# Kernel tuning notes

Hardware: AMD Instinct MI355X
Metric: run time of the kernel (lower is better)

Reference implementation:

```python
import jax, jax.numpy as jnp
import numpy as np

CLASSES = (32, 32)
SUPERCLASSES = 8
OVERALL = CLASSES[0] * CLASSES[1]
CLASS_FACTOR = OVERALL // SUPERCLASSES


def lrelu(x):
    return jax.nn.leaky_relu(x, 0.01)


def conv1x1(x, w, b):
    # x: [B,C,H,W], w: [O,C], b: [O]
    return jnp.einsum('oc,bchw->bohw', w, x) + b[None, :, None, None]


def cond_mul(x, inds, W, b):
    # x: [N,I], inds: [N] int, W: [K,I,O], b: [K,O]
    return jnp.einsum('ni,nio->no', x, W[inds]) + b[inds]


def setup_inputs() -> dict:
    key = jax.random.key(0)
    ks = jax.random.split(key, 24)
    s = 0.05
    d = {}
    d['x_in'] = jax.random.normal(ks[0], (1, 128, 192, 256), dtype=jnp.float32)
    # mask branch
    d['Wm1'] = jax.random.normal(ks[1], (32, 128)) * s
    d['bm1'] = jnp.zeros((32,), jnp.float32)
    d['Wm2'] = jax.random.normal(ks[2], (16, 32)) * s
    d['bm2'] = jnp.zeros((16,), jnp.float32)
    d['Wm3'] = jax.random.normal(ks[3], (1, 16)) * s
    d['bm3'] = jnp.zeros((1,), jnp.float32)
    # classification branch
    d['Wcl1'] = jax.random.normal(ks[4], (128, 128)) * s
    d['bcl1'] = jnp.zeros((128,), jnp.float32)
    d['Wcl21'] = jax.random.normal(ks[5], (128, 128)) * s
    d['bcl21'] = jnp.zeros((128,), jnp.float32)
    d['Wcl31'] = jax.random.normal(ks[6], (32, 128)) * s
    d['bcl31'] = jnp.zeros((32,), jnp.float32)
    d['Wcl22'] = jax.random.normal(ks[7], (CLASSES[0], 128, 32)) * s  # CondMul
    d['bcl22'] = jnp.zeros((CLASSES[0], 32), jnp.float32)
    d['Wcl32'] = jax.random.normal(ks[8], (CLASSES[0], 32, CLASSES[1])) * s
    d['bcl32'] = jnp.zeros((CLASSES[0], CLASSES[1]), jnp.float32)
    d['Wr1'] = jax.random.normal(ks[9], (128, 128)) * s
    d['br1'] = jnp.zeros((128,), jnp.float32)
    d['Wr2'] = jax.random.normal(ks[10], (SUPERCLASSES, 128, 32)) * s
    d['br2'] = jnp.zeros((SUPERCLASSES, 32), jnp.float32)
    d['Wr3'] = jax.random.normal(ks[11], (OVERALL, 32, 1)) * s
    d['br3'] = jnp.zeros((OVERALL, 1), jnp.float32)
    return d


def reference(x_in, Wm1, bm1, Wm2, bm2, Wm3, bm3,
              Wcl1, bcl1, Wcl21, bcl21, Wcl31, bcl31,
              Wcl22, bcl22, Wcl32, bcl32,
              Wr1, br1, Wr2, br2, Wr3, br3):
    B = x_in.shape[0]
    # mask branch
    m = lrelu(conv1x1(x_in, Wm1, bm1))
    m = lrelu(conv1x1(m, Wm2, bm2))
    mask = lrelu(conv1x1(m, Wm3, bm3))
    # classification branch
    x = lrelu(conv1x1(x_in, Wcl1, bcl1))          # [B,128,H,W]
    # torch: transpose(1,3) -> [B,W,H,C], flatten
    x_l = jnp.transpose(x, (0, 3, 2, 1)).reshape(-1, x.shape[1])
    x2 = lrelu(conv1x1(x, Wcl21, bcl21))
    cl1 = conv1x1(x2, Wcl31, bcl31)               # [B,classes0,H,W]
    inds1 = jnp.argmax(cl1, axis=1).reshape(-1).astype(jnp.int32)  # [N] (B,H,W order)
    h = lrelu(cond_mul(x_l, inds1, Wcl22, bcl22))  # [N,32]
    h = cond_mul(h, inds1, Wcl32, bcl32)           # [N,classes1]
    inds2 = jnp.argmax(h, axis=1).astype(jnp.int32)
    inds = inds1 * CLASSES[1] + inds2
    inds_r = jnp.clip(inds, 0, OVERALL - 1).astype(jnp.int32)
    inds_super = jnp.clip(inds_r // CLASS_FACTOR, 0, SUPERCLASSES - 1)
    r = lrelu(conv1x1(x_in, Wr1, br1))
    r_l = jnp.transpose(r, (0, 3, 2, 1)).reshape(-1, r.shape[1])
    r2 = lrelu(cond_mul(r_l, inds_super, Wr2, br2))  # [N,32]
    regression = cond_mul(r2, inds_r, Wr3, br3)      # [N,1]
    regression = regression.reshape(B, 1, 1, -1)
    inds = inds.reshape(regression.shape)
    x_real = (inds.astype(jnp.float32) + regression) * (1.0 / float(OVERALL))
    return (x_real, mask)
```

## Files before the change

### kernel.cpp

```cpp
#include <hip/hip_runtime.h>

#define HH 192
#define WW 256
#define NPIX (HH*WW)
#define NSEG (NPIX/64)

__device__ __forceinline__ float lrelu(float v) { return v > 0.0f ? v : 0.01f * v; }

__global__ __launch_bounds__(256, 3) void k_fused1(
    const float* __restrict__ X,
    const float* __restrict__ Wcl1, const float* __restrict__ bcl1,
    const float* __restrict__ Wr1,  const float* __restrict__ br1,
    const float* __restrict__ Wm1,  const float* __restrict__ bm1,
    const float* __restrict__ Wm2,  const float* __restrict__ bm2,
    const float* __restrict__ Wm3,  const float* __restrict__ bm3,
    float* __restrict__ x_t, float* __restrict__ r_t,
    float* __restrict__ out)
{
    __shared__ float As[16][132];
    __shared__ float Ws[16][132];
    __shared__ float m1buf[128][33];
    const int tid = threadIdx.x;
    const int q0  = blockIdx.x * 128;

    if (blockIdx.y == 2) {
        const int tc = tid & 31;
        const int tr = tid >> 5;
        float acc[4][4];
        #pragma unroll
        for (int i = 0; i < 4; ++i)
            #pragma unroll
            for (int j = 0; j < 4; ++j)
                acc[i][j] = bm1[tr * 4 + j];

        for (int k0 = 0; k0 < 128; k0 += 16) {
            #pragma unroll
            for (int p = 0; p < 2; ++p) {
                int lin = p * 1024 + tid * 4;
                int kk = lin >> 7, px = lin & 127;
                float4 v = *(const float4*)(X + (k0 + kk) * NPIX + q0 + px);
                *(float4*)(&As[kk][px]) = v;
            }
            if (tid < 128) {
                int row = tid >> 2, kc = (tid & 3) * 4;
                float4 v = *(const float4*)(Wm1 + row * 128 + k0 + kc);
                Ws[kc + 0][row] = v.x; Ws[kc + 1][row] = v.y;
                Ws[kc + 2][row] = v.z; Ws[kc + 3][row] = v.w;
            }
            __syncthreads();
            #pragma unroll
            for (int kk = 0; kk < 16; ++kk) {
                float4 a = *(const float4*)(&As[kk][tc * 4]);
                float4 w = *(const float4*)(&Ws[kk][tr * 4]);
                float av[4] = {a.x,a.y,a.z,a.w};
                float wv[4] = {w.x,w.y,w.z,w.w};
                #pragma unroll
                for (int i = 0; i < 4; ++i)
                    #pragma unroll
                    for (int j = 0; j < 4; ++j)
                        acc[i][j] = fmaf(av[i], wv[j], acc[i][j]);
            }
            __syncthreads();
        }
        #pragma unroll
        for (int i = 0; i < 4; ++i)
            #pragma unroll
            for (int j = 0; j < 4; ++j)
                m1buf[tc * 4 + i][tr * 4 + j] = lrelu(acc[i][j]);
        __syncthreads();
        if (tid < 128) {
            float m3 = bm3[0];
            #pragma unroll 2
            for (int j = 0; j < 16; ++j) {
                float s = bm2[j];
                #pragma unroll
                for (int k = 0; k < 32; ++k)
                    s = fmaf(Wm2[j * 32 + k], m1buf[tid][k], s);
                m3 = fmaf(Wm3[j], lrelu(s), m3);
            }
            out[NPIX + q0 + tid] = lrelu(m3);
        }
        return;
    }

    const float* __restrict__ W    = (blockIdx.y == 0) ? Wcl1 : Wr1;
    const float* __restrict__ bias = (blockIdx.y == 0) ? bcl1 : br1;
    float* __restrict__ outp       = (blockIdx.y == 0) ? x_t : r_t;

    const int tc = tid & 15;
    const int tr = tid >> 4;

    float acc[8][8];
    #pragma unroll
    for (int i = 0; i < 8; ++i)
        #pragma unroll
        for (int j = 0; j < 8; ++j)
            acc[i][j] = bias[(j >> 2) * 64 + tr * 4 + (j & 3)];

    for (int k0 = 0; k0 < 128; k0 += 16) {
        #pragma unroll
        for (int p = 0; p < 2; ++p) {
            int lin = p * 1024 + tid * 4;
            int kk = lin >> 7, px = lin & 127;
            float4 v = *(const float4*)(X + (k0 + kk) * NPIX + q0 + px);
            *(float4*)(&As[kk][px]) = v;
        }
        #pragma unroll
        for (int p = 0; p < 2; ++p) {
            int lin = p * 1024 + tid * 4;
            int row = lin >> 4, kc = lin & 15;
            float4 v = *(const float4*)(W + row * 128 + k0 + kc);
            Ws[kc + 0][row] = v.x; Ws[kc + 1][row] = v.y;
            Ws[kc + 2][row] = v.z; Ws[kc + 3][row] = v.w;
        }
        __syncthreads();
        #pragma unroll
        for (int kk = 0; kk < 16; ++kk) {
            float4 a0 = *(const float4*)(&As[kk][tc * 4]);
            float4 a1 = *(const float4*)(&As[kk][64 + tc * 4]);
            float4 w0 = *(const float4*)(&Ws[kk][tr * 4]);
            float4 w1 = *(const float4*)(&Ws[kk][64 + tr * 4]);
            float av[8] = {a0.x,a0.y,a0.z,a0.w,a1.x,a1.y,a1.z,a1.w};
            float wv[8] = {w0.x,w0.y,w0.z,w0.w,w1.x,w1.y,w1.z,w1.w};
            #pragma unroll
            for (int i = 0; i < 8; ++i)
                #pragma unroll
                for (int j = 0; j < 8; ++j)
                    acc[i][j] = fmaf(av[i], wv[j], acc[i][j]);
        }
        __syncthreads();
    }

    #pragma unroll
    for (int i = 0; i < 8; ++i) {
        int px = (i >> 2) * 64 + tc * 4 + (i & 3);
        int q  = q0 + px;
        int np = (q & 255) * 192 + (q >> 8);
        float* op = outp + (size_t)np * 128;
        #pragma unroll
        for (int jg = 0; jg < 2; ++jg) {
            float4 o;
            o.x = lrelu(acc[i][jg*4+0]); o.y = lrelu(acc[i][jg*4+1]);
            o.z = lrelu(acc[i][jg*4+2]); o.w = lrelu(acc[i][jg*4+3]);
            *(float4*)(op + jg * 64 + tr * 4) = o;
        }
    }
}

__global__ __launch_bounds__(256, 3) void k1b(
    const float* __restrict__ x_t,
    const float* __restrict__ Wcl21, const float* __restrict__ bcl21,
    const float* __restrict__ Wcl31, const float* __restrict__ bcl31,
    int* __restrict__ inds1_q)
{
    __shared__ float smem[8576];
    float (*As)[132]    = (float(*)[132])smem;
    float (*Ws)[132]    = (float(*)[132])(smem + 2112);
    float (*W31)[132]   = (float(*)[132])smem;
    float (*x2t)[68]    = (float(*)[68])(smem + 4224);
    float (*cl1buf)[33] = (float(*)[33])(smem + 4224);

    const int tid = threadIdx.x;
    const int n0  = blockIdx.x * 64;
    const int tcA = tid & 15, trA = tid >> 4;

    float acc[4][8];
    #pragma unroll
    for (int i = 0; i < 4; ++i)
        #pragma unroll
        for (int j = 0; j < 8; ++j)
            acc[i][j] = bcl21[(j >> 2) * 64 + trA * 4 + (j & 3)];

    for (int k0 = 0; k0 < 128; k0 += 16) {
        {
            int lin = tid * 4;
            int px = lin >> 4, kc = lin & 15;
            float4 v = *(const float4*)(x_t + (size_t)(n0 + px) * 128 + k0 + kc);
            As[kc + 0][px] = v.x; As[kc + 1][px] = v.y;
            As[kc + 2][px] = v.z; As[kc + 3][px] = v.w;
        }
        #pragma unroll
        for (int p = 0; p < 2; ++p) {
            int lin = p * 256 + tid;
            int r = lin >> 2, kc = (lin & 3) * 4;
            float4 v = *(const float4*)(Wcl21 + r * 128 + k0 + kc);
            Ws[kc + 0][r] = v.x; Ws[kc + 1][r] = v.y;
            Ws[kc + 2][r] = v.z; Ws[kc + 3][r] = v.w;
        }
        __syncthreads();
        #pragma unroll
        for (int kk = 0; kk < 16; ++kk) {
            float4 a  = *(const float4*)(&As[kk][tcA * 4]);
            float4 w0 = *(const float4*)(&Ws[kk][trA * 4]);
            float4 w1 = *(const float4*)(&Ws[kk][64 + trA * 4]);
            float av[4] = {a.x,a.y,a.z,a.w};
            float wv[8] = {w0.x,w0.y,w0.z,w0.w,w1.x,w1.y,w1.z,w1.w};
            #pragma unroll
            for (int i = 0; i < 4; ++i)
                #pragma unroll
                for (int j = 0; j < 8; ++j)
                    acc[i][j] = fmaf(av[i], wv[j], acc[i][j]);
        }
        __syncthreads();
    }

    const int tcB = tid & 15;
    const int trB = tid >> 4;
    float accB[4][2];
    #pragma unroll
    for (int i = 0; i < 4; ++i)
        #pragma unroll
        for (int j = 0; j < 2; ++j)
            accB[i][j] = bcl31[trB * 2 + j];

    #pragma unroll
    for (int p = 0; p < 4; ++p) {
        int lin = p * 1024 + tid * 4;
        int row = lin >> 7, kc = lin & 127;
        *(float4*)(&W31[row][kc]) = *(const float4*)(Wcl31 + row * 128 + kc);
    }
    #pragma unroll
    for (int j = 0; j < 4; ++j) {
        float4 o;
        o.x = lrelu(acc[0][j]); o.y = lrelu(acc[1][j]);
        o.z = lrelu(acc[2][j]); o.w = lrelu(acc[3][j]);
        *(float4*)(&x2t[trA * 4 + j][tcA * 4]) = o;
    }
    __syncthreads();
    for (int k = 0; k < 64; ++k) {
        float4 a = *(const float4*)(&x2t[k][tcB * 4]);
        float av[4] = {a.x,a.y,a.z,a.w};
        float w0 = W31[trB * 2 + 0][k];
        float w1 = W31[trB * 2 + 1][k];
        #pragma unroll
        for (int i = 0; i < 4; ++i) {
            accB[i][0] = fmaf(av[i], w0, accB[i][0]);
            accB[i][1] = fmaf(av[i], w1, accB[i][1]);
        }
    }
    __syncthreads();
    #pragma unroll
    for (int j = 0; j < 4; ++j) {
        float4 o;
        o.x = lrelu(acc[0][4+j]); o.y = lrelu(acc[1][4+j]);
        o.z = lrelu(acc[2][4+j]); o.w = lrelu(acc[3][4+j]);
        *(float4*)(&x2t[trA * 4 + j][tcA * 4]) = o;
    }
    __syncthreads();
    for (int k = 0; k < 64; ++k) {
        float4 a = *(const float4*)(&x2t[k][tcB * 4]);
        float av[4] = {a.x,a.y,a.z,a.w};
        float w0 = W31[trB * 2 + 0][64 + k];
        float w1 = W31[trB * 2 + 1][64 + k];
        #pragma unroll
        for (int i = 0; i < 4; ++i) {
            accB[i][0] = fmaf(av[i], w0, accB[i][0]);
            accB[i][1] = fmaf(av[i], w1, accB[i][1]);
        }
    }
    __syncthreads();

    #pragma unroll
    for (int i = 0; i < 4; ++i)
        #pragma unroll
        for (int j = 0; j < 2; ++j)
            cl1buf[tcB * 4 + i][trB * 2 + j] = accB[i][j];
    __syncthreads();
    if (tid < 64) {
        float bv = cl1buf[tid][0]; int bi = 0;
        #pragma unroll
        for (int c = 1; c < 32; ++c) {
            float v = cl1buf[tid][c];
            if (v > bv) { bv = v; bi = c; }
        }
        int n = n0 + tid;
        int w = n / 192, hh = n - w * 192;
        inds1_q[hh * 256 + w] = bi;
    }
}

__global__ void k_hist(const int* __restrict__ inds1_q, int* __restrict__ bh) {
    int tid = threadIdx.x;
    int n = blockIdx.x * 256 + tid;
    int key = inds1_q[n];
    int lane = tid & 63;
    int cnt = 0;
    for (int k = 0; k < 32; ++k) {
        unsigned long long m = __ballot(key == k);
        if (lane == k) cnt = __popcll(m);
    }
    if (lane < 32) bh[(n >> 6) * 32 + lane] = cnt;
}

__global__ void k_scanA(const int* __restrict__ bh, int* __restrict__ ebb,
                        int* __restrict__ total) {
    __shared__ int s[256];
    const int k = blockIdx.x, t = threadIdx.x;
    int v0 = bh[(t * 3 + 0) * 32 + k];
    int v1 = bh[(t * 3 + 1) * 32 + k];
    int v2 = bh[(t * 3 + 2) * 32 + k];
    int sum = v0 + v1 + v2;
    s[t] = sum; __syncthreads();
    for (int d = 1; d < 256; d <<= 1) {
        int x = (t >= d) ? s[t - d] : 0;
        __syncthreads();
        s[t] += x;
        __syncthreads();
    }
    int ex = s[t] - sum;
    ebb[(t * 3 + 0) * 32 + k] = ex;
    ebb[(t * 3 + 1) * 32 + k] = ex + v0;
    ebb[(t * 3 + 2) * 32 + k] = ex + v0 + v1;
    if (t == 255) total[k] = s[255];
}

__global__ void k_scatter2(const int* __restrict__ inds1_q,
                           const int* __restrict__ ebb,
                           const int* __restrict__ total,
                           int* __restrict__ order)
{
    __shared__ int ttot[32];
    const int tid = threadIdx.x;
    if (tid < 32) ttot[tid] = total[tid];
    __syncthreads();
    int n = blockIdx.x * 256 + tid;
    int key = inds1_q[n];
    int lane = tid & 63;
    unsigned long long peers = 0;
    for (int k = 0; k < 32; ++k) {
        unsigned long long m = __ballot(key == k);
        if (key == k) peers = m;
    }
    int rank = __popcll(peers & ((1ull << lane) - 1ull));
    int cbase = 0;
    #pragma unroll
    for (int k = 0; k < 32; ++k) cbase += (k < key) ? ttot[k] : 0;
    order[cbase + ebb[(n >> 6) * 32 + key] + rank] = n;
}

__global__ __launch_bounds__(256, 4) void k2h(
    const float* __restrict__ x_t,
    const float* __restrict__ Wcl22, const float* __restrict__ bcl22,
    const float* __restrict__ Wcl32, const float* __restrict__ bcl32,
    const int* __restrict__ total, const int* __restrict__ order,
    int* __restrict__ ind_ord)
{
    __shared__ float Was[4096];
    __shared__ float Wbs[1024];
    __shared__ int cpre[33];
    __shared__ int cbase[33];
    __shared__ int ttot[32];

    const int tid = threadIdx.x;
    if (tid < 32) ttot[tid] = total[tid];
    __syncthreads();
    if (tid == 0) {
        int s = 0, cb = 0;
        for (int k = 0; k < 32; ++k) {
            cpre[k] = s; cbase[k] = cb;
            int c = ttot[k];
            s += (c + 255) >> 8;
            cb += c;
        }
        cpre[32] = s; cbase[32] = cb;
    }
    __syncthreads();
    const int ci = blockIdx.x;
    if (ci >= cpre[32]) return;
    int cls = 0;
    while (cpre[cls + 1] <= ci) ++cls;
    const int st   = (ci - cpre[cls]) * 256;
    const int npx  = min(256, ttot[cls] - st);
    const int base = cbase[cls] + st;

    {
        const float4* ws = (const float4*)(Wcl22 + cls * 4096);
        #pragma unroll
        for (int j = 0; j < 4; ++j) ((float4*)Was)[j * 256 + tid] = ws[j * 256 + tid];
        ((float4*)Wbs)[tid] = ((const float4*)(Wcl32 + cls * 1024))[tid];
    }
    __syncthreads();

    const int m = order[base + min(tid, npx - 1)];
    const float4* xp = (const float4*)(x_t + (size_t)m * 128);

    float h[32];
    #pragma unroll
    for (int j = 0; j < 32; ++j) h[j] = bcl22[cls * 32 + j];
    #pragma unroll 2
    for (int c4 = 0; c4 < 32; ++c4) {
        float4 xv = xp[c4];
        float xa[4] = {xv.x, xv.y, xv.z, xv.w};
        #pragma unroll
        for (int cc = 0; cc < 4; ++cc) {
            const float* wr = &Was[(c4 * 4 + cc) * 32];
            #pragma unroll
            for (int j = 0; j < 32; ++j) h[j] = fmaf(xa[cc], wr[j], h[j]);
        }
    }
    #pragma unroll
    for (int j = 0; j < 32; ++j) h[j] = lrelu(h[j]);

    float g[32];
    #pragma unroll
    for (int j = 0; j < 32; ++j) g[j] = bcl32[cls * 32 + j];
    #pragma unroll 2
    for (int c = 0; c < 32; ++c) {
        float hv = h[c];
        const float* wr = &Wbs[c * 32];
        #pragma unroll
        for (int j = 0; j < 32; ++j) g[j] = fmaf(hv, wr[j], g[j]);
    }
    float bv = g[0]; int bi = 0;
    #pragma unroll
    for (int j = 1; j < 32; ++j)
        if (g[j] > bv) { bv = g[j]; bi = j; }
    if (tid < npx) ind_ord[base + tid] = cls * 32 + bi;
}

__global__ __launch_bounds__(256, 4) void k2r(
    const float* __restrict__ r_t,
    const float* __restrict__ Wr2,  const float* __restrict__ br2,
    const float* __restrict__ Wr3,  const float* __restrict__ br3,
    const int* __restrict__ total, const int* __restrict__ order,
    const int* __restrict__ ind_ord,
    float* __restrict__ out)
{
    __shared__ float Wcs[4096];
    __shared__ int cpre[33];
    __shared__ int cbase[33];
    __shared__ int ttot[32];

    const int tid = threadIdx.x;
    if (tid < 32) ttot[tid] = total[tid];
    __syncthreads();
    if (tid == 0) {
        int s = 0, cb = 0;
        for (int k = 0; k < 32; ++k) {
            cpre[k] = s; cbase[k] = cb;
            int c = ttot[k];
            s += (c + 255) >> 8;
            cb += c;
        }
        cpre[32] = s; cbase[32] = cb;
    }
    __syncthreads();
    const int ci = blockIdx.x;
    if (ci >= cpre[32]) return;
    int cls = 0;
    while (cpre[cls + 1] <= ci) ++cls;
    const int st   = (ci - cpre[cls]) * 256;
    const int npx  = min(256, ttot[cls] - st);
    const int base = cbase[cls] + st;
    const int sup  = cls >> 2;

    {
        const float4* ws = (const float4*)(Wr2 + sup * 4096);
        #pragma unroll
        for (int j = 0; j < 4; ++j) ((float4*)Wcs)[j * 256 + tid] = ws[j * 256 + tid];
    }
    __syncthreads();

    const int li  = min(tid, npx - 1);
    const int m   = order[base + li];
    const int ind = ind_ord[base + li];
    const float4* rp = (const float4*)(r_t + (size_t)m * 128);

    float r2[32];
    #pragma unroll
    for (int j = 0; j < 32; ++j) r2[j] = br2[sup * 32 + j];
    #pragma unroll 2
    for (int c4 = 0; c4 < 32; ++c4) {
        float4 rv = rp[c4];
        float ra[4] = {rv.x, rv.y, rv.z, rv.w};
        #pragma unroll
        for (int cc = 0; cc < 4; ++cc) {
            const float* wr = &Wcs[(c4 * 4 + cc) * 32];
            #pragma unroll
            for (int j = 0; j < 32; ++j) r2[j] = fmaf(ra[cc], wr[j], r2[j]);
        }
    }

    float reg = br3[ind];
    const float* __restrict__ w3 = Wr3 + ind * 32;
    #pragma unroll
    for (int j = 0; j < 32; ++j) reg = fmaf(lrelu(r2[j]), w3[j], reg);

    if (tid < npx) out[m] = ((float)ind + reg) * (1.0f / 1024.0f);
}

extern "C" void kernel_launch(void* const* d_in, const int* in_sizes, int n_in,
                              void* d_out, int out_size, void* d_ws, size_t ws_size,
                              hipStream_t stream)
{
    const float* X     = (const float*)d_in[0];
    const float* Wm1   = (const float*)d_in[1];
    const float* bm1   = (const float*)d_in[2];
    const float* Wm2   = (const float*)d_in[3];
    const float* bm2   = (const float*)d_in[4];
    const float* Wm3   = (const float*)d_in[5];
    const float* bm3   = (const float*)d_in[6];
    const float* Wcl1  = (const float*)d_in[7];
    const float* bcl1  = (const float*)d_in[8];
    const float* Wcl21 = (const float*)d_in[9];
    const float* bcl21 = (const float*)d_in[10];
    const float* Wcl31 = (const float*)d_in[11];
    const float* bcl31 = (const float*)d_in[12];
    const float* Wcl22 = (const float*)d_in[13];
    const float* bcl22 = (const float*)d_in[14];
    const float* Wcl32 = (const float*)d_in[15];
    const float* bcl32 = (const float*)d_in[16];
    const float* Wr1   = (const float*)d_in[17];
    const float* br1   = (const float*)d_in[18];
    const float* Wr2   = (const float*)d_in[19];
    const float* br2   = (const float*)d_in[20];
    const float* Wr3   = (const float*)d_in[21];
    const float* br3   = (const float*)d_in[22];
    float* out = (float*)d_out;

    float* x_t   = (float*)d_ws;
    float* r_t   = x_t + (size_t)NPIX * 128;
    int* inds1_q = (int*)(r_t + (size_t)NPIX * 128);
    int* order   = inds1_q + NPIX;
    int* ind_ord = order + NPIX;
    int* bh      = ind_ord + NPIX;
    int* ebb     = bh + NSEG * 32;
    int* total   = ebb + NSEG * 32;

    k_fused1<<<dim3(NPIX / 128, 3), 256, 0, stream>>>(X, Wcl1, bcl1, Wr1, br1,
                                                      Wm1, bm1, Wm2, bm2, Wm3, bm3,
                                                      x_t, r_t, out);
    k1b<<<NPIX / 64, 256, 0, stream>>>(x_t, Wcl21, bcl21, Wcl31, bcl31, inds1_q);
    k_hist<<<NPIX / 256, 256, 0, stream>>>(inds1_q, bh);
    k_scanA<<<32, 256, 0, stream>>>(bh, ebb, total);
    k_scatter2<<<NPIX / 256, 256, 0, stream>>>(inds1_q, ebb, total, order);
    k2h<<<224, 256, 0, stream>>>(x_t, Wcl22, bcl22, Wcl32, bcl32, total, order, ind_ord);
    k2r<<<224, 256, 0, stream>>>(r_t, Wr2, br2, Wr3, br3, total, order, ind_ord, out);
}
```

Before: 237.2 us.

## Merge histogram, scan, scatter and class kernels into one cooperative kernel

Measured after the change: 363.7 us. 1.53x slower.

```diff
diff --git a/kernel.cpp b/kernel.cpp
--- a/kernel.cpp
+++ b/kernel.cpp
@@ -1,4 +1,7 @@
 #include <hip/hip_runtime.h>
+#include <hip/hip_cooperative_groups.h>
+
+namespace cg = cooperative_groups;
 
 #define HH 192
 #define WW 256
@@ -279,214 +282,187 @@
     }
 }
 
-__global__ void k_hist(const int* __restrict__ inds1_q, int* __restrict__ bh) {
-    int tid = threadIdx.x;
-    int n = blockIdx.x * 256 + tid;
-    int key = inds1_q[n];
-    int lane = tid & 63;
-    int cnt = 0;
-    for (int k = 0; k < 32; ++k) {
-        unsigned long long m = __ballot(key == k);
-        if (lane == k) cnt = __popcll(m);
-    }
-    if (lane < 32) bh[(n >> 6) * 32 + lane] = cnt;
-}
-
-__global__ void k_scanA(const int* __restrict__ bh, int* __restrict__ ebb,
-                        int* __restrict__ total) {
-    __shared__ int s[256];
-    const int k = blockIdx.x, t = threadIdx.x;
-    int v0 = bh[(t * 3 + 0) * 32 + k];
-    int v1 = bh[(t * 3 + 1) * 32 + k];
-    int v2 = bh[(t * 3 + 2) * 32 + k];
-    int sum = v0 + v1 + v2;
-    s[t] = sum; __syncthreads();
-    for (int d = 1; d < 256; d <<= 1) {
-        int x = (t >= d) ? s[t - d] : 0;
-        __syncthreads();
-        s[t] += x;
-        __syncthreads();
-    }
-    int ex = s[t] - sum;
-    ebb[(t * 3 + 0) * 32 + k] = ex;
-    ebb[(t * 3 + 1) * 32 + k] = ex + v0;
-    ebb[(t * 3 + 2) * 32 + k] = ex + v0 + v1;
-    if (t == 255) total[k] = s[255];
-}
-
-__global__ void k_scatter2(const int* __restrict__ inds1_q,
-                           const int* __restrict__ ebb,
-                           const int* __restrict__ total,
-                           int* __restrict__ order)
-{
-    __shared__ int ttot[32];
-    const int tid = threadIdx.x;
-    if (tid < 32) ttot[tid] = total[tid];
-    __syncthreads();
-    int n = blockIdx.x * 256 + tid;
-    int key = inds1_q[n];
-    int lane = tid & 63;
-    unsigned long long peers = 0;
-    for (int k = 0; k < 32; ++k) {
-        unsigned long long m = __ballot(key == k);
-        if (key == k) peers = m;
-    }
-    int rank = __popcll(peers & ((1ull << lane) - 1ull));
-    int cbase = 0;
-    #pragma unroll
-    for (int k = 0; k < 32; ++k) cbase += (k < key) ? ttot[k] : 0;
-    order[cbase + ebb[(n >> 6) * 32 + key] + rank] = n;
-}
-
-__global__ __launch_bounds__(256, 4) void k2h(
+__global__ __launch_bounds__(256) void k_tail(
+    const int* __restrict__ inds1_q, int* __restrict__ bh,
+    int* __restrict__ ebb, int* __restrict__ total, int* __restrict__ order,
     const float* __restrict__ x_t,
     const float* __restrict__ Wcl22, const float* __restrict__ bcl22,
     const float* __restrict__ Wcl32, const float* __restrict__ bcl32,
-    const int* __restrict__ total, const int* __restrict__ order,
-    int* __restrict__ ind_ord)
-{
-    __shared__ float Was[4096];
-    __shared__ float Wbs[1024];
-    __shared__ int cpre[33];
-    __shared__ int cbase[33];
-    __shared__ int ttot[32];
-
-    const int tid = threadIdx.x;
-    if (tid < 32) ttot[tid] = total[tid];
-    __syncthreads();
-    if (tid == 0) {
-        int s = 0, cb = 0;
-        for (int k = 0; k < 32; ++k) {
-            cpre[k] = s; cbase[k] = cb;
-            int c = ttot[k];
-            s += (c + 255) >> 8;
-            cb += c;
-        }
-        cpre[32] = s; cbase[32] = cb;
-    }
-    __syncthreads();
-    const int ci = blockIdx.x;
-    if (ci >= cpre[32]) return;
-    int cls = 0;
-    while (cpre[cls + 1] <= ci) ++cls;
-    const int st   = (ci - cpre[cls]) * 256;
-    const int npx  = min(256, ttot[cls] - st);
-    const int base = cbase[cls] + st;
-
-    {
-        const float4* ws = (const float4*)(Wcl22 + cls * 4096);
-        #pragma unroll
-        for (int j = 0; j < 4; ++j) ((float4*)Was)[j * 256 + tid] = ws[j * 256 + tid];
-        ((float4*)Wbs)[tid] = ((const float4*)(Wcl32 + cls * 1024))[tid];
-    }
-    __syncthreads();
-
-    const int m = order[base + min(tid, npx - 1)];
-    const float4* xp = (const float4*)(x_t + (size_t)m * 128);
-
-    float h[32];
-    #pragma unroll
-    for (int j = 0; j < 32; ++j) h[j] = bcl22[cls * 32 + j];
-    #pragma unroll 2
-    for (int c4 = 0; c4 < 32; ++c4) {
-        float4 xv = xp[c4];
-        float xa[4] = {xv.x, xv.y, xv.z, xv.w};
-        #pragma unroll
-        for (int cc = 0; cc < 4; ++cc) {
-            const float* wr = &Was[(c4 * 4 + cc) * 32];
-            #pragma unroll
-            for (int j = 0; j < 32; ++j) h[j] = fmaf(xa[cc], wr[j], h[j]);
-        }
-    }
-    #pragma unroll
-    for (int j = 0; j < 32; ++j) h[j] = lrelu(h[j]);
-
-    float g[32];
-    #pragma unroll
-    for (int j = 0; j < 32; ++j) g[j] = bcl32[cls * 32 + j];
-    #pragma unroll 2
-    for (int c = 0; c < 32; ++c) {
-        float hv = h[c];
-        const float* wr = &Wbs[c * 32];
-        #pragma unroll
-        for (int j = 0; j < 32; ++j) g[j] = fmaf(hv, wr[j], g[j]);
-    }
-    float bv = g[0]; int bi = 0;
-    #pragma unroll
-    for (int j = 1; j < 32; ++j)
-        if (g[j] > bv) { bv = g[j]; bi = j; }
-    if (tid < npx) ind_ord[base + tid] = cls * 32 + bi;
-}
-
-__global__ __launch_bounds__(256, 4) void k2r(
+    int* __restrict__ ind_ord,
     const float* __restrict__ r_t,
     const float* __restrict__ Wr2,  const float* __restrict__ br2,
     const float* __restrict__ Wr3,  const float* __restrict__ br3,
-    const int* __restrict__ total, const int* __restrict__ order,
-    const int* __restrict__ ind_ord,
     float* __restrict__ out)
 {
-    __shared__ float Wcs[4096];
+    cg::grid_group grid = cg::this_grid();
+    const int tid = threadIdx.x;
+    const int bid = blockIdx.x;
+
+    __shared__ int s[256];
+    __shared__ int ttot[32];
     __shared__ int cpre[33];
     __shared__ int cbase[33];
-    __shared__ int ttot[32];
-
-    const int tid = threadIdx.x;
+    __shared__ float Wbuf[4096];
+    __shared__ float Wbs[1024];
+
+    if (bid < 192) {
+        int n = bid * 256 + tid;
+        int key = inds1_q[n];
+        int lane = tid & 63;
+        int cnt = 0;
+        for (int k = 0; k < 32; ++k) {
+            unsigned long long m = __ballot(key == k);
+            if (lane == k) cnt = __popcll(m);
+        }
+        if (lane < 32) bh[(n >> 6) * 32 + lane] = cnt;
+    }
+    grid.sync();
+
+    if (bid < 32) {
+        const int k = bid, t = tid;
+        int v0 = bh[(t * 3 + 0) * 32 + k];
+        int v1 = bh[(t * 3 + 1) * 32 + k];
+        int v2 = bh[(t * 3 + 2) * 32 + k];
+        int sum = v0 + v1 + v2;
+        s[t] = sum; __syncthreads();
+        for (int d = 1; d < 256; d <<= 1) {
+            int x = (t >= d) ? s[t - d] : 0;
+            __syncthreads();
+            s[t] += x;
+            __syncthreads();
+        }
+        int ex = s[t] - sum;
+        ebb[(t * 3 + 0) * 32 + k] = ex;
+        ebb[(t * 3 + 1) * 32 + k] = ex + v0;
+        ebb[(t * 3 + 2) * 32 + k] = ex + v0 + v1;
+        if (t == 255) total[k] = s[255];
+    }
+    grid.sync();
+
+    if (bid < 192) {
+        if (tid < 32) ttot[tid] = total[tid];
+        __syncthreads();
+        int n = bid * 256 + tid;
+        int key = inds1_q[n];
+        int lane = tid & 63;
+        unsigned long long peers = 0;
+        for (int k = 0; k < 32; ++k) {
+            unsigned long long m = __ballot(key == k);
+            if (key == k) peers = m;
+        }
+        int rank = __popcll(peers & ((1ull << lane) - 1ull));
+        int cbs = 0;
+        #pragma unroll
+        for (int k = 0; k < 32; ++k) cbs += (k < key) ? ttot[k] : 0;
+        order[cbs + ebb[(n >> 6) * 32 + key] + rank] = n;
+    }
+    grid.sync();
+
     if (tid < 32) ttot[tid] = total[tid];
     __syncthreads();
     if (tid == 0) {
-        int s = 0, cb = 0;
+        int sc = 0, cb = 0;
         for (int k = 0; k < 32; ++k) {
-            cpre[k] = s; cbase[k] = cb;
+            cpre[k] = sc; cbase[k] = cb;
             int c = ttot[k];
-            s += (c + 255) >> 8;
+            sc += (c + 255) >> 8;
             cb += c;
         }
-        cpre[32] = s; cbase[32] = cb;
-    }
-    __syncthreads();
-    const int ci = blockIdx.x;
-    if (ci >= cpre[32]) return;
-    int cls = 0;
-    while (cpre[cls + 1] <= ci) ++cls;
-    const int st   = (ci - cpre[cls]) * 256;
-    const int npx  = min(256, ttot[cls] - st);
-    const int base = cbase[cls] + st;
-    const int sup  = cls >> 2;
-
-    {
-        const float4* ws = (const float4*)(Wr2 + sup * 4096);
-        #pragma unroll
-        for (int j = 0; j < 4; ++j) ((float4*)Wcs)[j * 256 + tid] = ws[j * 256 + tid];
-    }
-    __syncthreads();
-
-    const int li  = min(tid, npx - 1);
-    const int m   = order[base + li];
-    const int ind = ind_ord[base + li];
-    const float4* rp = (const float4*)(r_t + (size_t)m * 128);
-
-    float r2[32];
-    #pragma unroll
-    for (int j = 0; j < 32; ++j) r2[j] = br2[sup * 32 + j];
-    #pragma unroll 2
-    for (int c4 = 0; c4 < 32; ++c4) {
-        float4 rv = rp[c4];
-        float ra[4] = {rv.x, rv.y, rv.z, rv.w};
-        #pragma unroll
-        for (int cc = 0; cc < 4; ++cc) {
-            const float* wr = &Wcs[(c4 * 4 + cc) * 32];
-            #pragma unroll
-            for (int j = 0; j < 32; ++j) r2[j] = fmaf(ra[cc], wr[j], r2[j]);
-        }
-    }
-
-    float reg = br3[ind];
-    const float* __restrict__ w3 = Wr3 + ind * 32;
-    #pragma unroll
-    for (int j = 0; j < 32; ++j) reg = fmaf(lrelu(r2[j]), w3[j], reg);
-
-    if (tid < npx) out[m] = ((float)ind + reg) * (1.0f / 1024.0f);
+        cpre[32] = sc; cbase[32] = cb;
+    }
+    __syncthreads();
+    const bool act = (bid < cpre[32]);
+    int cls = 0, st = 0, npx = 1, base = 0;
+    if (act) {
+        while (cpre[cls + 1] <= bid) ++cls;
+        st   = (bid - cpre[cls]) * 256;
+        npx  = min(256, ttot[cls] - st);
+        base = cbase[cls] + st;
+    }
+    const int sup = cls >> 2;
+
+    if (act) {
+        {
+            const float4* ws = (const float4*)(Wcl22 + cls * 4096);
+            #pragma unroll
+            for (int j = 0; j < 4; ++j) ((float4*)Wbuf)[j * 256 + tid] = ws[j * 256 + tid];
+            ((float4*)Wbs)[tid] = ((const float4*)(Wcl32 + cls * 1024))[tid];
+        }
+        __syncthreads();
+
+        const int m = order[base + min(tid, npx - 1)];
+        const float4* xp = (const float4*)(x_t + (size_t)m * 128);
+
+        float h[32];
+        #pragma unroll
+        for (int j = 0; j < 32; ++j) h[j] = bcl22[cls * 32 + j];
+        #pragma unroll 2
+        for (int c4 = 0; c4 < 32; ++c4) {
+            float4 xv = xp[c4];
+            float xa[4] = {xv.x, xv.y, xv.z, xv.w};
+            #pragma unroll
+            for (int cc = 0; cc < 4; ++cc) {
+                const float* wr = &Wbuf[(c4 * 4 + cc) * 32];
+                #pragma unroll
+                for (int j = 0; j < 32; ++j) h[j] = fmaf(xa[cc], wr[j], h[j]);
+            }
+        }
+        #pragma unroll
+        for (int j = 0; j < 32; ++j) h[j] = lrelu(h[j]);
+
+        float g[32];
+        #pragma unroll
+        for (int j = 0; j < 32; ++j) g[j] = bcl32[cls * 32 + j];
+        #pragma unroll 2
+        for (int c = 0; c < 32; ++c) {
+            float hv = h[c];
+            const float* wr = &Wbs[c * 32];
+            #pragma unroll
+            for (int j = 0; j < 32; ++j) g[j] = fmaf(hv, wr[j], g[j]);
+        }
+        float bv = g[0]; int bi = 0;
+        #pragma unroll
+        for (int j = 1; j < 32; ++j)
+            if (g[j] > bv) { bv = g[j]; bi = j; }
+        if (tid < npx) ind_ord[base + tid] = cls * 32 + bi;
+    }
+    grid.sync();
+
+    if (act) {
+        {
+            const float4* ws = (const float4*)(Wr2 + sup * 4096);
+            #pragma unroll
+            for (int j = 0; j < 4; ++j) ((float4*)Wbuf)[j * 256 + tid] = ws[j * 256 + tid];
+        }
+        __syncthreads();
+
+        const int li  = min(tid, npx - 1);
+        const int m   = order[base + li];
+        const int ind = ind_ord[base + li];
+        const float4* rp = (const float4*)(r_t + (size_t)m * 128);
+
+        float r2[32];
+        #pragma unroll
+        for (int j = 0; j < 32; ++j) r2[j] = br2[sup * 32 + j];
+        #pragma unroll 2
+        for (int c4 = 0; c4 < 32; ++c4) {
+            float4 rv = rp[c4];
+            float ra[4] = {rv.x, rv.y, rv.z, rv.w};
+            #pragma unroll
+            for (int cc = 0; cc < 4; ++cc) {
+                const float* wr = &Wbuf[(c4 * 4 + cc) * 32];
+                #pragma unroll
+                for (int j = 0; j < 32; ++j) r2[j] = fmaf(ra[cc], wr[j], r2[j]);
+            }
+        }
+
+        float reg = br3[ind];
+        const float* __restrict__ w3 = Wr3 + ind * 32;
+        #pragma unroll
+        for (int j = 0; j < 32; ++j) reg = fmaf(lrelu(r2[j]), w3[j], reg);
+
+        if (tid < npx) out[m] = ((float)ind + reg) * (1.0f / 1024.0f);
+    }
 }
 
 extern "C" void kernel_launch(void* const* d_in, const int* in_sizes, int n_in,
@@ -531,9 +507,13 @@
                                                       Wm1, bm1, Wm2, bm2, Wm3, bm3,
                                                       x_t, r_t, out);
     k1b<<<NPIX / 64, 256, 0, stream>>>(x_t, Wcl21, bcl21, Wcl31, bcl31, inds1_q);
-    k_hist<<<NPIX / 256, 256, 0, stream>>>(inds1_q, bh);
-    k_scanA<<<32, 256, 0, stream>>>(bh, ebb, total);
-    k_scatter2<<<NPIX / 256, 256, 0, stream>>>(inds1_q, ebb, total, order);
-    k2h<<<224, 256, 0, stream>>>(x_t, Wcl22, bcl22, Wcl32, bcl32, total, order, ind_ord);
-    k2r<<<224, 256, 0, stream>>>(r_t, Wr2, br2, Wr3, br3, total, order, ind_ord, out);
+
+    void* args[] = {
+        (void*)&inds1_q, (void*)&bh, (void*)&ebb, (void*)&total, (void*)&order,
+        (void*)&x_t, (void*)&Wcl22, (void*)&bcl22, (void*)&Wcl32, (void*)&bcl32,
+        (void*)&ind_ord, (void*)&r_t, (void*)&Wr2, (void*)&br2, (void*)&Wr3,
+        (void*)&br3, (void*)&out
+    };
+    hipLaunchCooperativeKernel(reinterpret_cast<void*>(k_tail),
+                               dim3(224), dim3(256), args, 0, stream);
 }
```

## Use split-bf16 MFMA for the regression-branch 1x1 conv in fused kernel

Applied to the files above, without the earlier changes.

Result: faster. 230.7 us (-2.7%).

```diff
diff --git a/kernel.cpp b/kernel.cpp
--- a/kernel.cpp
+++ b/kernel.cpp
@@ -6,6 +6,17 @@
 #define NSEG (NPIX/64)
 
 __device__ __forceinline__ float lrelu(float v) { return v > 0.0f ? v : 0.01f * v; }
+
+__device__ __forceinline__ unsigned short bfhi(float x) {
+    unsigned b = __float_as_uint(x);
+    return (unsigned short)((b + 0x7FFFu + ((b >> 16) & 1u)) >> 16);
+}
+__device__ __forceinline__ float bff(unsigned short u) {
+    return __uint_as_float(((unsigned)u) << 16);
+}
+
+typedef __attribute__((ext_vector_type(8))) short short8v;
+typedef __attribute__((ext_vector_type(4))) float f32x4;
 
 __global__ __launch_bounds__(256, 3) void k_fused1(
     const float* __restrict__ X,
@@ -17,9 +28,11 @@
     float* __restrict__ x_t, float* __restrict__ r_t,
     float* __restrict__ out)
 {
-    __shared__ float As[16][132];
-    __shared__ float Ws[16][132];
-    __shared__ float m1buf[128][33];
+    __shared__ float smem[10240];
+    float (*As)[132]   = (float(*)[132])smem;
+    float (*Ws)[132]   = (float(*)[132])(smem + 2112);
+    float (*m1buf)[33] = (float(*)[33])(smem + 4224);
+
     const int tid = threadIdx.x;
     const int q0  = blockIdx.x * 128;
 
@@ -83,9 +96,110 @@
         return;
     }
 
-    const float* __restrict__ W    = (blockIdx.y == 0) ? Wcl1 : Wr1;
-    const float* __restrict__ bias = (blockIdx.y == 0) ? bcl1 : br1;
-    float* __restrict__ outp       = (blockIdx.y == 0) ? x_t : r_t;
+    if (blockIdx.y == 1) {
+        unsigned short* Whi  = (unsigned short*)smem;
+        unsigned short* Wlo  = Whi  + 5120;
+        unsigned short* Xthi = Wlo  + 5120;
+        unsigned short* Xtlo = Xthi + 5120;
+
+        const int l = tid & 63;
+        const int w = tid >> 6;
+        const int c = l & 15;
+        const int g = l >> 4;
+        const int o0 = w * 32;
+
+        float bv[2][4];
+        #pragma unroll
+        for (int ot = 0; ot < 2; ++ot)
+            #pragma unroll
+            for (int r = 0; r < 4; ++r)
+                bv[ot][r] = br1[o0 + ot * 16 + g * 4 + r];
+
+        f32x4 acc[2][8];
+        #pragma unroll
+        for (int ot = 0; ot < 2; ++ot)
+            #pragma unroll
+            for (int pt = 0; pt < 8; ++pt) {
+                acc[ot][pt][0] = bv[ot][0]; acc[ot][pt][1] = bv[ot][1];
+                acc[ot][pt][2] = bv[ot][2]; acc[ot][pt][3] = bv[ot][3];
+            }
+
+        for (int k0 = 0; k0 < 128; k0 += 32) {
+            #pragma unroll
+            for (int p = 0; p < 4; ++p) {
+                int lin = p * 1024 + tid * 4;
+                int kk = lin >> 7, px = lin & 127;
+                float4 v = *(const float4*)(X + (size_t)(k0 + kk) * NPIX + q0 + px);
+                float xv[4] = {v.x, v.y, v.z, v.w};
+                #pragma unroll
+                for (int i = 0; i < 4; ++i) {
+                    unsigned short h = bfhi(xv[i]);
+                    int idx = (px + i) * 40 + kk;
+                    Xthi[idx] = h;
+                    Xtlo[idx] = bfhi(xv[i] - bff(h));
+                }
+            }
+            #pragma unroll
+            for (int p = 0; p < 4; ++p) {
+                int lin = p * 1024 + tid * 4;
+                int o = lin >> 5, kc = lin & 31;
+                float4 v = *(const float4*)(Wr1 + o * 128 + k0 + kc);
+                float wv[4] = {v.x, v.y, v.z, v.w};
+                #pragma unroll
+                for (int i = 0; i < 4; ++i) {
+                    unsigned short h = bfhi(wv[i]);
+                    int idx = o * 40 + kc + i;
+                    Whi[idx] = h;
+                    Wlo[idx] = bfhi(wv[i] - bff(h));
+                }
+            }
+            __syncthreads();
+
+            short8v ahi[2], alo[2];
+            #pragma unroll
+            for (int ot = 0; ot < 2; ++ot) {
+                int ao = (o0 + ot * 16 + c) * 40 + g * 8;
+                ahi[ot] = *(const short8v*)(Whi + ao);
+                alo[ot] = *(const short8v*)(Wlo + ao);
+            }
+            #pragma unroll
+            for (int pt = 0; pt < 8; ++pt) {
+                int bo = (pt * 16 + c) * 40 + g * 8;
+                short8v bhi = *(const short8v*)(Xthi + bo);
+                short8v blo = *(const short8v*)(Xtlo + bo);
+                #pragma unroll
+                for (int ot = 0; ot < 2; ++ot) {
+                    acc[ot][pt] = __builtin_amdgcn_mfma_f32_16x16x32_bf16(
+                        ahi[ot], bhi, acc[ot][pt], 0, 0, 0);
+                    acc[ot][pt] = __builtin_amdgcn_mfma_f32_16x16x32_bf16(
+                        ahi[ot], blo, acc[ot][pt], 0, 0, 0);
+                    acc[ot][pt] = __builtin_amdgcn_mfma_f32_16x16x32_bf16(
+                        alo[ot], bhi, acc[ot][pt], 0, 0, 0);
+                }
+            }
+            __syncthreads();
+        }
+
+        #pragma unroll
+        for (int pt = 0; pt < 8; ++pt) {
+            int px = pt * 16 + c;
+            int q  = q0 + px;
+            int np = (q & 255) * 192 + (q >> 8);
+            float* op = r_t + (size_t)np * 128;
+            #pragma unroll
+            for (int ot = 0; ot < 2; ++ot) {
+                float4 o4;
+                o4.x = lrelu(acc[ot][pt][0]); o4.y = lrelu(acc[ot][pt][1]);
+                o4.z = lrelu(acc[ot][pt][2]); o4.w = lrelu(acc[ot][pt][3]);
+                *(float4*)(op + o0 + ot * 16 + g * 4) = o4;
+            }
+        }
+        return;
+    }
+
+    const float* __restrict__ W    = Wcl1;
+    const float* __restrict__ bias = bcl1;
+    float* __restrict__ outp       = x_t;
 
     const int tc = tid & 15;
     const int tr = tid >> 4;
```
